# Kernel optimization log

Measured on AMD Instinct MI355X. Metric: run time of the kernel, lower is better.

Reference implementation:

```python
import jax, jax.numpy as jnp
import numpy as np

NEG_SLOPE = 0.2


def _gat_layer(x, W, a_src, a_dst, b, src, dst, n_nodes, heads, dim):
    # x: [N, F_in]; W: [F_in, heads*dim]
    h = (x @ W).reshape(n_nodes, heads, dim)            # [N,H,D]
    e_src = (h * a_src).sum(-1)                          # [N,H]
    e_dst = (h * a_dst).sum(-1)                          # [N,H]
    e = jax.nn.leaky_relu(e_src[src] + e_dst[dst], NEG_SLOPE)  # [E,H]
    # edge softmax over incoming edges of each target node
    m = jax.ops.segment_max(e, dst, num_segments=n_nodes)      # [N,H]
    ex = jnp.exp(e - m[dst])
    denom = jax.ops.segment_sum(ex, dst, num_segments=n_nodes)  # [N,H]
    alpha = ex / denom[dst]                              # [E,H]
    out = jax.ops.segment_sum(h[src] * alpha[:, :, None], dst,
                              num_segments=n_nodes)      # [N,H,D]
    return out.reshape(n_nodes, heads * dim) + b


def setup_inputs() -> dict:
    key = jax.random.key(0)
    ks = jax.random.split(key, 10)
    N, E, F_in = 100000, 1600000, 300
    x = jax.random.normal(ks[0], (N, F_in), dtype=jnp.float32)
    edge_index = jax.random.randint(ks[1], (2, E), 0, N, dtype=jnp.int64)
    s = 0.1
    return {
        'x': x,
        'edge_index': edge_index,
        'W1': jax.random.normal(ks[2], (F_in, 64), jnp.float32) * s,
        'att_src1': jax.random.normal(ks[3], (8, 8), jnp.float32) * s,
        'att_dst1': jax.random.normal(ks[4], (8, 8), jnp.float32) * s,
        'b1': jax.random.normal(ks[5], (64,), jnp.float32) * s,
        'W2': jax.random.normal(ks[6], (64, 64), jnp.float32) * s,
        'att_src2': jax.random.normal(ks[7], (1, 64), jnp.float32) * s,
        'att_dst2': jax.random.normal(ks[8], (1, 64), jnp.float32) * s,
        'b2': jax.random.normal(ks[9], (64,), jnp.float32) * s,
    }


def reference(x, edge_index, W1, att_src1, att_dst1, b1, W2, att_src2, att_dst2, b2):
    N = x.shape[0]
    # add self-loops (PyG GATConv default)
    loop = jnp.arange(N, dtype=edge_index.dtype)
    src = jnp.concatenate([edge_index[0], loop])
    dst = jnp.concatenate([edge_index[1], loop])
    # dropout p=0.6 is identity in eval mode
    h = _gat_layer(x, W1, att_src1, att_dst1, b1, src, dst, N, 8, 8)    # [N,64]
    h = jax.nn.elu(h)
    h = _gat_layer(h, W2, att_src2, att_dst2, b2, src, dst, N, 1, 64)   # [N,64]
    return jax.nn.log_softmax(h, axis=1)
```

## Files before the change

### kernel.cpp

```cpp
#include <hip/hip_runtime.h>
#include <math.h>

using short8  = __attribute__((ext_vector_type(8))) short;
using ushort8 = __attribute__((ext_vector_type(8))) unsigned short;
using f32x4   = __attribute__((ext_vector_type(4))) float;

#define NBLKS 512
#define BPAD  800
#define EB 8

__device__ __forceinline__ unsigned short f2bf(float f) {
    unsigned u = __float_as_uint(f);
    unsigned r = u + 0x7FFF + ((u >> 16) & 1);
    return (unsigned short)(r >> 16);
}
__device__ __forceinline__ float bf2f(unsigned short v) {
    return __uint_as_float((unsigned)v << 16);
}


__global__ void detect64_kernel(const int* __restrict__ ei, int E, int* __restrict__ flag) {
    __shared__ int any;
    if (threadIdx.x == 0) any = 0;
    __syncthreads();
    for (int i = threadIdx.x; i < 1024; i += 256) {
        if (ei[2 * i + 1] != 0) { any = 1; break; }
    }
    __syncthreads();
    if (threadIdx.x == 0) *flag = (any ? 0 : 1);
}


__global__ __launch_bounds__(256) void binA_kernel(
    const int* __restrict__ ei, int E, int N, const int* __restrict__ flag,
    int nbuck, int* __restrict__ hist, int chunk) {
    __shared__ int lh[BPAD];
    for (int i = threadIdx.x; i < nbuck; i += 256) lh[i] = 0;
    __syncthreads();
    int is64 = *flag;
    int Etot = E + N;
    int beg = blockIdx.x * chunk, end = min(Etot, beg + chunk);
    for (int i = beg + threadIdx.x; i < end; i += 256) {
        int d = (i < E) ? (is64 ? ei[2 * (E + i)] : ei[E + i]) : (i - E);
        atomicAdd(&lh[d >> 7], 1);
    }
    __syncthreads();
    for (int i = threadIdx.x; i < nbuck; i += 256) hist[blockIdx.x * BPAD + i] = lh[i];
}

__global__ void scanBlocks_kernel(int* __restrict__ hist, int nbuck, int* __restrict__ bucketTotal) {
    int bin = blockIdx.x * 256 + threadIdx.x;
    if (bin >= nbuck) return;
    int run = 0;
    for (int b = 0; b < NBLKS; b++) {
        int v = hist[b * BPAD + bin];
        hist[b * BPAD + bin] = run;
        run += v;
    }
    bucketTotal[bin] = run;
}

__global__ void scanBucket_kernel(const int* __restrict__ bucketTotal, int nbuck,
                                  int* __restrict__ bucketBase) {
    __shared__ int s[1024];
    int t = threadIdx.x;
    int v = (t < nbuck) ? bucketTotal[t] : 0;
    s[t] = v;
    __syncthreads();
    for (int off = 1; off < 1024; off <<= 1) {
        int x = (t >= off) ? s[t - off] : 0;
        __syncthreads();
        s[t] += x;
        __syncthreads();
    }
    if (t < nbuck) bucketBase[t] = s[t] - v;
    if (t == nbuck - 1) bucketBase[nbuck] = s[t];
}

__global__ __launch_bounds__(256) void binB_kernel(
    const int* __restrict__ ei, int E, int N, const int* __restrict__ flag,
    int nbuck, const int* __restrict__ hist, const int* __restrict__ bucketBase,
    int* __restrict__ tmp, int chunk) {
    __shared__ int cur[BPAD];
    for (int i = threadIdx.x; i < nbuck; i += 256)
        cur[i] = bucketBase[i] + hist[blockIdx.x * BPAD + i];
    __syncthreads();
    int is64 = *flag;
    int Etot = E + N;
    int beg = blockIdx.x * chunk, end = min(Etot, beg + chunk);
    for (int i = beg + threadIdx.x; i < end; i += 256) {
        int s, d;
        if (i < E) {
            if (is64) { s = ei[2 * i]; d = ei[2 * (E + i)]; }
            else      { s = ei[i];     d = ei[E + i]; }
        } else { s = i - E; d = i - E; }
        int pos = atomicAdd(&cur[d >> 7], 1);
        tmp[pos] = ((d & 127) << 17) | s;
    }
}

__global__ __launch_bounds__(256) void binC_kernel(
    const int* __restrict__ tmp, const int* __restrict__ bucketBase, int nbuck,
    int N, int Etot, int* __restrict__ rowptr, int* __restrict__ col) {
    __shared__ int lh[128];
    __shared__ int cur[128];
    int g = blockIdx.x;
    int t = threadIdx.x;
    int beg = bucketBase[g], end = bucketBase[g + 1];
    if (t < 128) lh[t] = 0;
    __syncthreads();
    for (int i = beg + t; i < end; i += 256) atomicAdd(&lh[tmp[i] >> 17], 1);
    __syncthreads();
    int c = (t < 128) ? lh[t] : 0;
    for (int off = 1; off < 128; off <<= 1) {
        int x = 0;
        if (t < 128 && t >= off) x = lh[t - off];
        __syncthreads();
        if (t < 128) lh[t] += x;
        __syncthreads();
    }
    if (t < 128) {
        int excl = lh[t] - c;
        cur[t] = beg + excl;
        int node = g * 128 + t;
        if (node < N) rowptr[node] = beg + excl;
    }
    if (g == 0 && t == 0) rowptr[N] = Etot;
    if (g == 0 && t < 16) col[Etot + t] = 0;
    __syncthreads();
    for (int i = beg + t; i < end; i += 256) {
        int v = tmp[i];
        int pos = atomicAdd(&cur[v >> 17], 1);
        col[pos] = v & 0x1FFFF;
    }
}


__global__ __launch_bounds__(256) void gemm1_mfma_kernel(
    const float* __restrict__ x, const float* __restrict__ W,
    const float* __restrict__ asrc, const float* __restrict__ adst,
    unsigned short* __restrict__ hbf, float* __restrict__ es, float* __restrict__ ed, int N) {
    __shared__ __align__(16) unsigned short A_lds[128 * 40];
    __shared__ __align__(16) unsigned short B_lds[64 * 40];
    const int tx = threadIdx.x;
    const int wv = tx >> 6;
    const int lane = tx & 63;
    const int l15 = lane & 15;
    const int quad = lane >> 4;
    const int rowBase = blockIdx.x * 128;

    f32x4 acc[2][4];
#pragma unroll
    for (int rt = 0; rt < 2; rt++)
#pragma unroll
        for (int ct = 0; ct < 4; ct++) acc[rt][ct] = (f32x4){0.f, 0.f, 0.f, 0.f};

    const int kq = tx & 7;
    const int r0 = tx >> 3;
    const int colB = tx & 63;
    const int kkb = (tx >> 6) * 8;

    for (int k0 = 0; k0 < 320; k0 += 32) {
        bool kvalid = (k0 + kq * 4 + 4 <= 300);
#pragma unroll
        for (int p = 0; p < 4; p++) {
            int row = p * 32 + r0;
            int grow = rowBase + row;
            float4 v = make_float4(0.f, 0.f, 0.f, 0.f);
            if (kvalid && grow < N) v = *(const float4*)&x[(size_t)grow * 300 + k0 + kq * 4];
            *(ushort4*)&A_lds[row * 40 + kq * 4] =
                make_ushort4(f2bf(v.x), f2bf(v.y), f2bf(v.z), f2bf(v.w));
        }
        {
            unsigned short t0, t1, t2, t3, t4, t5, t6, t7;
            float v;
            v = (k0 + kkb + 0 < 300) ? W[(size_t)(k0 + kkb + 0) * 64 + colB] : 0.f; t0 = f2bf(v);
            v = (k0 + kkb + 1 < 300) ? W[(size_t)(k0 + kkb + 1) * 64 + colB] : 0.f; t1 = f2bf(v);
            v = (k0 + kkb + 2 < 300) ? W[(size_t)(k0 + kkb + 2) * 64 + colB] : 0.f; t2 = f2bf(v);
            v = (k0 + kkb + 3 < 300) ? W[(size_t)(k0 + kkb + 3) * 64 + colB] : 0.f; t3 = f2bf(v);
            v = (k0 + kkb + 4 < 300) ? W[(size_t)(k0 + kkb + 4) * 64 + colB] : 0.f; t4 = f2bf(v);
            v = (k0 + kkb + 5 < 300) ? W[(size_t)(k0 + kkb + 5) * 64 + colB] : 0.f; t5 = f2bf(v);
            v = (k0 + kkb + 6 < 300) ? W[(size_t)(k0 + kkb + 6) * 64 + colB] : 0.f; t6 = f2bf(v);
            v = (k0 + kkb + 7 < 300) ? W[(size_t)(k0 + kkb + 7) * 64 + colB] : 0.f; t7 = f2bf(v);
            *(ushort4*)&B_lds[colB * 40 + kkb]     = make_ushort4(t0, t1, t2, t3);
            *(ushort4*)&B_lds[colB * 40 + kkb + 4] = make_ushort4(t4, t5, t6, t7);
        }
        __syncthreads();
        short8 af[2], bfr[4];
#pragma unroll
        for (int rt = 0; rt < 2; rt++)
            af[rt] = *(const short8*)&A_lds[(wv * 32 + rt * 16 + l15) * 40 + quad * 8];
#pragma unroll
        for (int ct = 0; ct < 4; ct++)
            bfr[ct] = *(const short8*)&B_lds[(ct * 16 + l15) * 40 + quad * 8];
#pragma unroll
        for (int rt = 0; rt < 2; rt++)
#pragma unroll
            for (int ct = 0; ct < 4; ct++)
                acc[rt][ct] = __builtin_amdgcn_mfma_f32_16x16x32_bf16(af[rt], bfr[ct], acc[rt][ct], 0, 0, 0);
        __syncthreads();
    }

    float as_v[4], ad_v[4];
#pragma unroll
    for (int ct = 0; ct < 4; ct++) {
        as_v[ct] = asrc[ct * 16 + l15];
        ad_v[ct] = adst[ct * 16 + l15];
    }
#pragma unroll
    for (int rt = 0; rt < 2; rt++) {
#pragma unroll
        for (int reg = 0; reg < 4; reg++) {
            int row = rowBase + wv * 32 + rt * 16 + quad * 4 + reg;
            bool ok = (row < N);
#pragma unroll
            for (int ct = 0; ct < 4; ct++) {
                float v = acc[rt][ct][reg];
                if (ok) hbf[(size_t)row * 64 + ct * 16 + l15] = f2bf(v);
                float ps = v * as_v[ct];
                float pd = v * ad_v[ct];
                ps += __shfl_xor(ps, 1); ps += __shfl_xor(ps, 2); ps += __shfl_xor(ps, 4);
                pd += __shfl_xor(pd, 1); pd += __shfl_xor(pd, 2); pd += __shfl_xor(pd, 4);
                if ((lane & 7) == 0 && ok) {
                    int head = 2 * ct + ((lane >> 3) & 1);
                    es[row * 8 + head] = ps;
                    ed[row * 8 + head] = pd;
                }
            }
        }
    }
}


__global__ __launch_bounds__(256) void gemm2_mfma_kernel(
    const unsigned short* __restrict__ xin, const float* __restrict__ W,
    const float* __restrict__ asrc, const float* __restrict__ adst,
    unsigned short* __restrict__ hbf, float* __restrict__ es, float* __restrict__ ed, int N) {
    __shared__ __align__(16) unsigned short A_lds[128 * 72];
    __shared__ __align__(16) unsigned short B_lds[64 * 72];
    const int tx = threadIdx.x;
    const int wv = tx >> 6;
    const int lane = tx & 63;
    const int l15 = lane & 15;
    const int quad = lane >> 4;
    const int rowBase = blockIdx.x * 128;

    f32x4 acc[2][4];
#pragma unroll
    for (int rt = 0; rt < 2; rt++)
#pragma unroll
        for (int ct = 0; ct < 4; ct++) acc[rt][ct] = (f32x4){0.f, 0.f, 0.f, 0.f};

    {
        int colB = tx & 63;
        int kk = (tx >> 6) * 16;
#pragma unroll
        for (int j = 0; j < 16; j++)
            B_lds[colB * 72 + kk + j] = f2bf(W[(size_t)(kk + j) * 64 + colB]);
    }
    {
        int kq = tx & 7, r0 = tx >> 3;
        const ushort8 z = (ushort8){0, 0, 0, 0, 0, 0, 0, 0};
#pragma unroll
        for (int p = 0; p < 4; p++) {
            int row = p * 32 + r0;
            int grow = rowBase + row;
            ushort8 v = z;
            if (grow < N) v = *(const ushort8*)&xin[(size_t)grow * 64 + kq * 8];
            *(ushort8*)&A_lds[row * 72 + kq * 8] = v;
        }
    }
    __syncthreads();
#pragma unroll
    for (int c = 0; c < 2; c++) {
        short8 af[2], bfr[4];
#pragma unroll
        for (int rt = 0; rt < 2; rt++)
            af[rt] = *(const short8*)&A_lds[(wv * 32 + rt * 16 + l15) * 72 + quad * 8 + c * 32];
#pragma unroll
        for (int ct = 0; ct < 4; ct++)
            bfr[ct] = *(const short8*)&B_lds[(ct * 16 + l15) * 72 + quad * 8 + c * 32];
#pragma unroll
        for (int rt = 0; rt < 2; rt++)
#pragma unroll
            for (int ct = 0; ct < 4; ct++)
                acc[rt][ct] = __builtin_amdgcn_mfma_f32_16x16x32_bf16(af[rt], bfr[ct], acc[rt][ct], 0, 0, 0);
    }

    float as_v[4], ad_v[4];
#pragma unroll
    for (int ct = 0; ct < 4; ct++) {
        as_v[ct] = asrc[ct * 16 + l15];
        ad_v[ct] = adst[ct * 16 + l15];
    }
#pragma unroll
    for (int rt = 0; rt < 2; rt++) {
#pragma unroll
        for (int reg = 0; reg < 4; reg++) {
            int row = rowBase + wv * 32 + rt * 16 + quad * 4 + reg;
            bool ok = (row < N);
            float ps = 0.f, pd = 0.f;
#pragma unroll
            for (int ct = 0; ct < 4; ct++) {
                float v = acc[rt][ct][reg];
                if (ok) hbf[(size_t)row * 64 + ct * 16 + l15] = f2bf(v);
                ps = fmaf(v, as_v[ct], ps);
                pd = fmaf(v, ad_v[ct], pd);
            }
            ps += __shfl_xor(ps, 1); ps += __shfl_xor(ps, 2);
            ps += __shfl_xor(ps, 4); ps += __shfl_xor(ps, 8);
            pd += __shfl_xor(pd, 1); pd += __shfl_xor(pd, 2);
            pd += __shfl_xor(pd, 4); pd += __shfl_xor(pd, 8);
            if (l15 == 0 && ok) { es[row] = ps; ed[row] = pd; }
        }
    }
}


__global__ __launch_bounds__(256) void alpha1_kernel(
    const int* __restrict__ rowptr, const int* __restrict__ col,
    const float* __restrict__ es, const float* __restrict__ ed,
    unsigned short* __restrict__ w1a, float* __restrict__ rden, int N) {
    int tid = blockIdx.x * 256 + threadIdx.x;
    int node = tid >> 3, head = tid & 7;
    if (node >= N) return;
    int beg = rowptr[node], end = rowptr[node + 1];
    float edv = ed[node * 8 + head];
    float l = 0.f;
    for (int e = beg; e < end; e++) {
        int s = col[e];
        float v = es[s * 8 + head] + edv;
        v = (v > 0.f) ? v : 0.2f * v;
        v = fminf(v, 30.f);
        float wj = __expf(v);
        l += wj;
        w1a[e * 8 + head] = f2bf(wj);
    }
    rden[node * 8 + head] = 1.f / l;
}

__global__ __launch_bounds__(256) void alpha2_kernel(
    const int* __restrict__ rowptr, const int* __restrict__ col,
    const float* __restrict__ es, const float* __restrict__ ed,
    float* __restrict__ w2a, float* __restrict__ rden, int N) {
    int node = blockIdx.x * 256 + threadIdx.x;
    if (node >= N) return;
    int beg = rowptr[node], end = rowptr[node + 1];
    float edv = ed[node];
    float l = 0.f;
    for (int e = beg; e < end; e++) {
        float v = es[col[e]] + edv;
        v = (v > 0.f) ? v : 0.2f * v;
        v = fminf(v, 30.f);
        float wj = __expf(v);
        l += wj;
        w2a[e] = wj;
    }
    rden[node] = 1.f / l;
}


__global__ __launch_bounds__(256) void agg1g_kernel(
    const int* __restrict__ rowptr, const int* __restrict__ col,
    const unsigned short* __restrict__ hbf, const unsigned short* __restrict__ w1a,
    const float* __restrict__ rden, const float* __restrict__ b,
    unsigned int* __restrict__ outbf, int N) {
    int node = blockIdx.x * 4 + (threadIdx.x >> 6);
    int lane = threadIdx.x & 63;
    if (node >= N) return;
    int half = lane >> 5, fl = lane & 31;
    int f0 = fl * 2, hh = fl >> 2;
    int beg = rowptr[node], end = rowptr[node + 1];
    float rinv = rden[node * 8 + hh];
    float acc0 = 0.f, acc1 = 0.f;
    for (int i = beg; i < end; i += 16) {
        int ei_[EB], ss[EB];
        float wv[EB];
        unsigned hp[EB];
#pragma unroll
        for (int j = 0; j < EB; j++) ei_[j] = i + 2 * j + half;
#pragma unroll
        for (int j = 0; j < EB; j++) ss[j] = col[ei_[j]];
#pragma unroll
        for (int j = 0; j < EB; j++) wv[j] = bf2f(w1a[ei_[j] * 8 + hh]);
#pragma unroll
        for (int j = 0; j < EB; j++) hp[j] = *(const unsigned*)&hbf[(size_t)ss[j] * 64 + f0];
#pragma unroll
        for (int j = 0; j < EB; j++) wv[j] = (ei_[j] < end) ? wv[j] : 0.f;
#pragma unroll
        for (int j = 0; j < EB; j++) {
            float lo = __uint_as_float(hp[j] << 16);
            float hi = __uint_as_float(hp[j] & 0xFFFF0000u);
            acc0 = fmaf(wv[j], lo, acc0);
            acc1 = fmaf(wv[j], hi, acc1);
        }
    }
    acc0 += __shfl_xor(acc0, 32);
    acc1 += __shfl_xor(acc1, 32);
    float o0 = acc0 * rinv + b[f0];
    float o1 = acc1 * rinv + b[f0 + 1];
    o0 = (o0 > 0.f) ? o0 : expm1f(o0);
    o1 = (o1 > 0.f) ? o1 : expm1f(o1);
    if (half == 0) {
        unsigned pk = (unsigned)f2bf(o0) | ((unsigned)f2bf(o1) << 16);
        outbf[((size_t)node * 64 + f0) >> 1] = pk;
    }
}

__global__ __launch_bounds__(256) void agg2g_kernel(
    const int* __restrict__ rowptr, const int* __restrict__ col,
    const unsigned short* __restrict__ hbf, const float* __restrict__ w2a,
    const float* __restrict__ rden, const float* __restrict__ b,
    float* __restrict__ out, int N) {
    int node = blockIdx.x * 4 + (threadIdx.x >> 6);
    int lane = threadIdx.x & 63;
    if (node >= N) return;
    int half = lane >> 5, fl = lane & 31;
    int f0 = fl * 2;
    int beg = rowptr[node], end = rowptr[node + 1];
    float rinv = rden[node];
    float acc0 = 0.f, acc1 = 0.f;
    for (int i = beg; i < end; i += 16) {
        int ei_[EB], ss[EB];
        float wv[EB];
        unsigned hp[EB];
#pragma unroll
        for (int j = 0; j < EB; j++) ei_[j] = i + 2 * j + half;
#pragma unroll
        for (int j = 0; j < EB; j++) ss[j] = col[ei_[j]];
#pragma unroll
        for (int j = 0; j < EB; j++) wv[j] = w2a[ei_[j]];
#pragma unroll
        for (int j = 0; j < EB; j++) hp[j] = *(const unsigned*)&hbf[(size_t)ss[j] * 64 + f0];
#pragma unroll
        for (int j = 0; j < EB; j++) wv[j] = (ei_[j] < end) ? wv[j] : 0.f;
#pragma unroll
        for (int j = 0; j < EB; j++) {
            float lo = __uint_as_float(hp[j] << 16);
            float hi = __uint_as_float(hp[j] & 0xFFFF0000u);
            acc0 = fmaf(wv[j], lo, acc0);
            acc1 = fmaf(wv[j], hi, acc1);
        }
    }
    acc0 += __shfl_xor(acc0, 32);
    acc1 += __shfl_xor(acc1, 32);
    float o0 = acc0 * rinv + b[f0];
    float o1 = acc1 * rinv + b[f0 + 1];
    float M = fmaxf(o0, o1);
    M = fmaxf(M, __shfl_xor(M, 1));  M = fmaxf(M, __shfl_xor(M, 2));
    M = fmaxf(M, __shfl_xor(M, 4));  M = fmaxf(M, __shfl_xor(M, 8));
    M = fmaxf(M, __shfl_xor(M, 16));
    float se = __expf(o0 - M) + __expf(o1 - M);
    se += __shfl_xor(se, 1);  se += __shfl_xor(se, 2);
    se += __shfl_xor(se, 4);  se += __shfl_xor(se, 8);
    se += __shfl_xor(se, 16);
    float ls = logf(se);
    if (half == 0) {
        float2 r = make_float2(o0 - M - ls, o1 - M - ls);
        *(float2*)&out[(size_t)node * 64 + f0] = r;
    }
}


extern "C" void kernel_launch(void* const* d_in, const int* in_sizes, int n_in,
                              void* d_out, int out_size, void* d_ws, size_t ws_size,
                              hipStream_t stream) {
    const float* x   = (const float*)d_in[0];
    const int*   ei  = (const int*)d_in[1];
    const float* W1  = (const float*)d_in[2];
    const float* as1 = (const float*)d_in[3];
    const float* ad1 = (const float*)d_in[4];
    const float* b1  = (const float*)d_in[5];
    const float* W2  = (const float*)d_in[6];
    const float* as2 = (const float*)d_in[7];
    const float* ad2 = (const float*)d_in[8];
    const float* b2  = (const float*)d_in[9];
    const int N = in_sizes[0] / 300;
    const int E = in_sizes[1] / 2;
    const int Etot = E + N;
    const int nbuck = (N + 127) >> 7;
    (void)n_in; (void)out_size; (void)ws_size;

    char* w = (char*)d_ws;
    auto alloc = [&](size_t bytes) -> char* {
        char* p = w;
        w += (bytes + 255) & ~(size_t)255;
        return p;
    };
    int*   flag        = (int*)alloc(256);
    int*   hist        = (int*)alloc((size_t)NBLKS * BPAD * 4);
    int*   bucketTotal = (int*)alloc((size_t)(BPAD + 1) * 4);
    int*   bucketBase  = (int*)alloc((size_t)(BPAD + 1) * 4);
    int*   tmp         = (int*)alloc((size_t)(Etot + 16) * 4);
    int*   rowptr      = (int*)alloc((size_t)(N + 1) * 4);
    int*   col         = (int*)alloc((size_t)(Etot + 16) * 4);
    unsigned short* h1  = (unsigned short*)alloc((size_t)N * 64 * 2);
    unsigned short* h1p = (unsigned short*)alloc((size_t)N * 64 * 2);
    float* es1         = (float*)alloc((size_t)N * 8 * 4);
    float* ed1         = (float*)alloc((size_t)N * 8 * 4);
    float* es2         = (float*)alloc((size_t)N * 4);
    float* ed2         = (float*)alloc((size_t)N * 4);
    unsigned short* w1a = (unsigned short*)alloc((size_t)(Etot + 16) * 8 * 2);
    float* rden1       = (float*)alloc((size_t)N * 8 * 4);
    float* rden2       = (float*)alloc((size_t)N * 4);
    unsigned short* h2 = h1;
    float* w2a = (float*)tmp;

    detect64_kernel<<<1, 256, 0, stream>>>(ei, E, flag);

    int chunk = (Etot + NBLKS - 1) / NBLKS;
    binA_kernel<<<NBLKS, 256, 0, stream>>>(ei, E, N, flag, nbuck, hist, chunk);
    scanBlocks_kernel<<<(nbuck + 255) / 256, 256, 0, stream>>>(hist, nbuck, bucketTotal);
    scanBucket_kernel<<<1, 1024, 0, stream>>>(bucketTotal, nbuck, bucketBase);
    binB_kernel<<<NBLKS, 256, 0, stream>>>(ei, E, N, flag, nbuck, hist, bucketBase, tmp, chunk);
    binC_kernel<<<nbuck, 256, 0, stream>>>(tmp, bucketBase, nbuck, N, Etot, rowptr, col);

    gemm1_mfma_kernel<<<(N + 127) / 128, 256, 0, stream>>>(x, W1, as1, ad1, h1, es1, ed1, N);
    alpha1_kernel<<<(N * 8 + 255) / 256, 256, 0, stream>>>(rowptr, col, es1, ed1, w1a, rden1, N);
    agg1g_kernel<<<(N + 3) / 4, 256, 0, stream>>>(rowptr, col, h1, w1a, rden1, b1,
                                                  (unsigned int*)h1p, N);
    gemm2_mfma_kernel<<<(N + 127) / 128, 256, 0, stream>>>(h1p, W2, as2, ad2, h2, es2, ed2, N);
    alpha2_kernel<<<(N + 255) / 256, 256, 0, stream>>>(rowptr, col, es2, ed2, w2a, rden2, N);
    agg2g_kernel<<<(N + 3) / 4, 256, 0, stream>>>(rowptr, col, h2, w2a, rden2, b2, (float*)d_out, N);
}
```

Baseline: 479.5 us.

## Fuse edge-softmax weight computation into aggregation kernels for both GAT layers

Removes the separate alpha1/alpha2 kernels, which wrote per-edge exponentiated attention weights and per-node reciprocal denominators to global memory. The aggregation kernels now gather es for each source node, apply leaky-relu and exp inline, and accumulate the denominator alongside the weighted feature sum. This drops two kernel launches and the write-then-read of per-edge weight arrays. In exchange each aggregation lane does extra exp work and an extra gather of es per edge, and exp is computed redundantly across lanes that share a head.

```diff
diff --git a/kernel.cpp b/kernel.cpp
--- a/kernel.cpp
+++ b/kernel.cpp
@@ -317,53 +317,10 @@
 }
 
 
-__global__ __launch_bounds__(256) void alpha1_kernel(
+__global__ __launch_bounds__(256) void agg1f_kernel(
     const int* __restrict__ rowptr, const int* __restrict__ col,
-    const float* __restrict__ es, const float* __restrict__ ed,
-    unsigned short* __restrict__ w1a, float* __restrict__ rden, int N) {
-    int tid = blockIdx.x * 256 + threadIdx.x;
-    int node = tid >> 3, head = tid & 7;
-    if (node >= N) return;
-    int beg = rowptr[node], end = rowptr[node + 1];
-    float edv = ed[node * 8 + head];
-    float l = 0.f;
-    for (int e = beg; e < end; e++) {
-        int s = col[e];
-        float v = es[s * 8 + head] + edv;
-        v = (v > 0.f) ? v : 0.2f * v;
-        v = fminf(v, 30.f);
-        float wj = __expf(v);
-        l += wj;
-        w1a[e * 8 + head] = f2bf(wj);
-    }
-    rden[node * 8 + head] = 1.f / l;
-}
-
-__global__ __launch_bounds__(256) void alpha2_kernel(
-    const int* __restrict__ rowptr, const int* __restrict__ col,
-    const float* __restrict__ es, const float* __restrict__ ed,
-    float* __restrict__ w2a, float* __restrict__ rden, int N) {
-    int node = blockIdx.x * 256 + threadIdx.x;
-    if (node >= N) return;
-    int beg = rowptr[node], end = rowptr[node + 1];
-    float edv = ed[node];
-    float l = 0.f;
-    for (int e = beg; e < end; e++) {
-        float v = es[col[e]] + edv;
-        v = (v > 0.f) ? v : 0.2f * v;
-        v = fminf(v, 30.f);
-        float wj = __expf(v);
-        l += wj;
-        w2a[e] = wj;
-    }
-    rden[node] = 1.f / l;
-}
-
-
-__global__ __launch_bounds__(256) void agg1g_kernel(
-    const int* __restrict__ rowptr, const int* __restrict__ col,
-    const unsigned short* __restrict__ hbf, const unsigned short* __restrict__ w1a,
-    const float* __restrict__ rden, const float* __restrict__ b,
+    const unsigned short* __restrict__ hbf, const float* __restrict__ es,
+    const float* __restrict__ ed, const float* __restrict__ b,
     unsigned int* __restrict__ outbf, int N) {
     int node = blockIdx.x * 4 + (threadIdx.x >> 6);
     int lane = threadIdx.x & 63;
@@ -371,32 +328,37 @@
     int half = lane >> 5, fl = lane & 31;
     int f0 = fl * 2, hh = fl >> 2;
     int beg = rowptr[node], end = rowptr[node + 1];
-    float rinv = rden[node * 8 + hh];
-    float acc0 = 0.f, acc1 = 0.f;
+    float edv = ed[node * 8 + hh];
+    float acc0 = 0.f, acc1 = 0.f, lsum = 0.f;
     for (int i = beg; i < end; i += 16) {
         int ei_[EB], ss[EB];
-        float wv[EB];
+        float ev[EB];
         unsigned hp[EB];
 #pragma unroll
         for (int j = 0; j < EB; j++) ei_[j] = i + 2 * j + half;
 #pragma unroll
         for (int j = 0; j < EB; j++) ss[j] = col[ei_[j]];
 #pragma unroll
-        for (int j = 0; j < EB; j++) wv[j] = bf2f(w1a[ei_[j] * 8 + hh]);
+        for (int j = 0; j < EB; j++) ev[j] = es[ss[j] * 8 + hh];
 #pragma unroll
         for (int j = 0; j < EB; j++) hp[j] = *(const unsigned*)&hbf[(size_t)ss[j] * 64 + f0];
 #pragma unroll
-        for (int j = 0; j < EB; j++) wv[j] = (ei_[j] < end) ? wv[j] : 0.f;
-#pragma unroll
         for (int j = 0; j < EB; j++) {
+            float e = ev[j] + edv;
+            e = (e > 0.f) ? e : 0.2f * e;
+            float wj = __expf(fminf(e, 30.f));
+            wj = (ei_[j] < end) ? wj : 0.f;
+            lsum += wj;
             float lo = __uint_as_float(hp[j] << 16);
             float hi = __uint_as_float(hp[j] & 0xFFFF0000u);
-            acc0 = fmaf(wv[j], lo, acc0);
-            acc1 = fmaf(wv[j], hi, acc1);
+            acc0 = fmaf(wj, lo, acc0);
+            acc1 = fmaf(wj, hi, acc1);
         }
     }
     acc0 += __shfl_xor(acc0, 32);
     acc1 += __shfl_xor(acc1, 32);
+    lsum += __shfl_xor(lsum, 32);
+    float rinv = 1.f / lsum;
     float o0 = acc0 * rinv + b[f0];
     float o1 = acc1 * rinv + b[f0 + 1];
     o0 = (o0 > 0.f) ? o0 : expm1f(o0);
@@ -407,10 +369,10 @@
     }
 }
 
-__global__ __launch_bounds__(256) void agg2g_kernel(
+__global__ __launch_bounds__(256) void agg2f_kernel(
     const int* __restrict__ rowptr, const int* __restrict__ col,
-    const unsigned short* __restrict__ hbf, const float* __restrict__ w2a,
-    const float* __restrict__ rden, const float* __restrict__ b,
+    const unsigned short* __restrict__ hbf, const float* __restrict__ es,
+    const float* __restrict__ ed, const float* __restrict__ b,
     float* __restrict__ out, int N) {
     int node = blockIdx.x * 4 + (threadIdx.x >> 6);
     int lane = threadIdx.x & 63;
@@ -418,32 +380,37 @@
     int half = lane >> 5, fl = lane & 31;
     int f0 = fl * 2;
     int beg = rowptr[node], end = rowptr[node + 1];
-    float rinv = rden[node];
-    float acc0 = 0.f, acc1 = 0.f;
+    float edv = ed[node];
+    float acc0 = 0.f, acc1 = 0.f, lsum = 0.f;
     for (int i = beg; i < end; i += 16) {
         int ei_[EB], ss[EB];
-        float wv[EB];
+        float ev[EB];
         unsigned hp[EB];
 #pragma unroll
         for (int j = 0; j < EB; j++) ei_[j] = i + 2 * j + half;
 #pragma unroll
         for (int j = 0; j < EB; j++) ss[j] = col[ei_[j]];
 #pragma unroll
-        for (int j = 0; j < EB; j++) wv[j] = w2a[ei_[j]];
+        for (int j = 0; j < EB; j++) ev[j] = es[ss[j]];
 #pragma unroll
         for (int j = 0; j < EB; j++) hp[j] = *(const unsigned*)&hbf[(size_t)ss[j] * 64 + f0];
 #pragma unroll
-        for (int j = 0; j < EB; j++) wv[j] = (ei_[j] < end) ? wv[j] : 0.f;
-#pragma unroll
         for (int j = 0; j < EB; j++) {
+            float e = ev[j] + edv;
+            e = (e > 0.f) ? e : 0.2f * e;
+            float wj = __expf(fminf(e, 30.f));
+            wj = (ei_[j] < end) ? wj : 0.f;
+            lsum += wj;
             float lo = __uint_as_float(hp[j] << 16);
             float hi = __uint_as_float(hp[j] & 0xFFFF0000u);
-            acc0 = fmaf(wv[j], lo, acc0);
-            acc1 = fmaf(wv[j], hi, acc1);
+            acc0 = fmaf(wj, lo, acc0);
+            acc1 = fmaf(wj, hi, acc1);
         }
     }
     acc0 += __shfl_xor(acc0, 32);
     acc1 += __shfl_xor(acc1, 32);
+    lsum += __shfl_xor(lsum, 32);
+    float rinv = 1.f / lsum;
     float o0 = acc0 * rinv + b[f0];
     float o1 = acc1 * rinv + b[f0 + 1];
     float M = fmaxf(o0, o1);
@@ -500,11 +467,7 @@
     float* ed1         = (float*)alloc((size_t)N * 8 * 4);
     float* es2         = (float*)alloc((size_t)N * 4);
     float* ed2         = (float*)alloc((size_t)N * 4);
-    unsigned short* w1a = (unsigned short*)alloc((size_t)(Etot + 16) * 8 * 2);
-    float* rden1       = (float*)alloc((size_t)N * 8 * 4);
-    float* rden2       = (float*)alloc((size_t)N * 4);
     unsigned short* h2 = h1;
-    float* w2a = (float*)tmp;
 
     detect64_kernel<<<1, 256, 0, stream>>>(ei, E, flag);
 
@@ -516,10 +479,8 @@
     binC_kernel<<<nbuck, 256, 0, stream>>>(tmp, bucketBase, nbuck, N, Etot, rowptr, col);
 
     gemm1_mfma_kernel<<<(N + 127) / 128, 256, 0, stream>>>(x, W1, as1, ad1, h1, es1, ed1, N);
-    alpha1_kernel<<<(N * 8 + 255) / 256, 256, 0, stream>>>(rowptr, col, es1, ed1, w1a, rden1, N);
-    agg1g_kernel<<<(N + 3) / 4, 256, 0, stream>>>(rowptr, col, h1, w1a, rden1, b1,
+    agg1f_kernel<<<(N + 3) / 4, 256, 0, stream>>>(rowptr, col, h1, es1, ed1, b1,
                                                   (unsigned int*)h1p, N);
     gemm2_mfma_kernel<<<(N + 127) / 128, 256, 0, stream>>>(h1p, W2, as2, ad2, h2, es2, ed2, N);
-    alpha2_kernel<<<(N + 255) / 256, 256, 0, stream>>>(rowptr, col, es2, ed2, w2a, rden2, N);
-    agg2g_kernel<<<(N + 3) / 4, 256, 0, stream>>>(rowptr, col, h2, w2a, rden2, b2, (float*)d_out, N);
-}
+    agg2f_kernel<<<(N + 3) / 4, 256, 0, stream>>>(rowptr, col, h2, es2, ed2, b2, (float*)d_out, N);
+}
```

Result: faster. 437.5 us (-8.8%).
